# Performance work log

Hardware: AMD Instinct MI355X
Metric: run time of the kernel (lower is better)

## Reference

```python
import jax, jax.numpy as jnp
import numpy as np


def setup_inputs() -> dict:
    key = jax.random.key(0)
    k1, k2 = jax.random.split(key)
    B, N, M = 4, 16384, 4096
    src_points = jax.random.normal(k1, (B, N, 3), dtype=jnp.float32)
    target_verts = jax.random.normal(k2, (B, M, 3), dtype=jnp.float32)
    return {"src_points": src_points, "target_verts": target_verts}


def reference(src_points, target_verts):
    # target_faces=None path of ChamferLoss: degenerate one-vertex triangles,
    # so closest-point-on-mesh == nearest target vertex.
    # d2[b,n,m] = ||p_bn - v_bm||^2 via the expansion p2 + v2 - 2 p.v
    p2 = jnp.sum(src_points * src_points, axis=-1)          # (B, N)
    v2 = jnp.sum(target_verts * target_verts, axis=-1)      # (B, M)
    pv = jnp.einsum('bnd,bmd->bnm', src_points, target_verts)  # (B, N, M)
    d2 = p2[:, :, None] + v2[:, None, :] - 2.0 * pv
    d2 = jnp.maximum(d2, 0.0)
    min_d2 = jnp.min(d2, axis=-1)                            # (B, N)
    num_src_per_batch = src_points.shape[1]
    loss = jnp.sum(min_d2, axis=-1) / num_src_per_batch      # (B,)
    return loss
```

## Files before the change

### kernel.cpp

```cpp
#include <hip/hip_runtime.h>
#include <float.h>


typedef __bf16 bf16x8 __attribute__((ext_vector_type(8)));
typedef float  f32x16 __attribute__((ext_vector_type(16)));

constexpr int B = 4, N = 16384, M = 4096;
constexpr int BN = B * N;
constexpr int NCHUNK = 4;
constexpr int CHUNK_V = M / NCHUNK;
constexpr int TILES = CHUNK_V / 32;
constexpr int TPB = 256;
constexpr int PPB = 128;
constexpr int PBLK = BN / PPB;
constexpr size_t BFRAG_BYTES = (size_t)B * M * 32;

__global__ __launch_bounds__(256) void chamfer_pre(
    const float* __restrict__ tv, unsigned char* __restrict__ bfr,
    float* __restrict__ out)
{
    if (blockIdx.x == 0 && threadIdx.x < B) out[threadIdx.x] = 0.0f;
    int i = blockIdx.x * 256 + threadIdx.x;
    int b = i >> 12;
    int m = i & (M - 1);
    float x = tv[3 * i + 0], y = tv[3 * i + 1], z = tv[3 * i + 2];
    __bf16 xh = (__bf16)x, yh = (__bf16)y, zh = (__bf16)z;
    float xhf = (float)xh, yhf = (float)yh, zhf = (float)zh;
    __bf16 xl = (__bf16)(x - xhf), yl = (__bf16)(y - yhf), zl = (__bf16)(z - zhf);
    float v2 = fmaf(x, x, fmaf(y, y, z * z));
    __bf16 v2h = (__bf16)v2;
    __bf16 v2l = (__bf16)(v2 - (float)v2h);
    __bf16 zero = (__bf16)0.0f;

    bf16x8 h0, h1;
    h0[0] = (__bf16)(-2.0f * xhf); h0[1] = (__bf16)(-2.0f * yhf);
    h0[2] = (__bf16)(-2.0f * zhf);
    h0[3] = h0[0]; h0[4] = h0[1]; h0[5] = h0[2];
    h0[6] = (__bf16)(-2.0f * (float)xl); h0[7] = (__bf16)(-2.0f * (float)yl);
    h1[0] = (__bf16)(-2.0f * (float)zl); h1[1] = v2h; h1[2] = v2l;
    h1[3] = zero; h1[4] = zero; h1[5] = zero; h1[6] = zero; h1[7] = zero;

    int chunk = m >> 10, local = m & (CHUNK_V - 1), tile = local >> 5, c = m & 31;
    size_t base = (size_t)b * 131072 + (size_t)chunk * 32768 + tile * 1024 + c * 16;
    *(bf16x8*)(bfr + base)       = h0;
    *(bf16x8*)(bfr + base + 512) = h1;
}

__global__ __launch_bounds__(TPB, 4) void chamfer_mfma(
    const float* __restrict__ src, const unsigned char* __restrict__ bfr,
    float* __restrict__ partial)
{
    __shared__ uint4 lds4[2048];
    const char* ldsc = (const char*)lds4;
    const int blk   = blockIdx.x;
    const int chunk = blk & 3;
    const int pblk  = blk >> 2;
    const int b     = pblk >> 7;
    const int t     = threadIdx.x;
    const int w     = t >> 6, L = t & 63;
    const int half  = L >> 5, c = L & 31;

    const uint4* gsrc = (const uint4*)(bfr + (size_t)b * 131072 + (size_t)chunk * 32768);
#pragma unroll
    for (int i = 0; i < 8; ++i) lds4[i * 256 + t] = gsrc[i * 256 + t];

    const int gp = pblk * PPB + w * 32 + c;
    float ax = src[3*gp], ay = src[3*gp+1], az = src[3*gp+2];
    __bf16 one = (__bf16)1.0f, zero = (__bf16)0.0f;
    bf16x8 aA;
    {
        __bf16 xh=(__bf16)ax, yh=(__bf16)ay, zh=(__bf16)az;
        __bf16 xl=(__bf16)(ax-(float)xh), yl=(__bf16)(ay-(float)yh), zl=(__bf16)(az-(float)zh);
        if (half == 0) { aA[0]=xh; aA[1]=yh; aA[2]=zh; aA[3]=xl; aA[4]=yl; aA[5]=zl; aA[6]=xh; aA[7]=yh; }
        else { aA[0]=zh; aA[1]=one; aA[2]=one; aA[3]=zero; aA[4]=zero; aA[5]=zero; aA[6]=zero; aA[7]=zero; }
    }

    f32x16 mn, zeroC;
#pragma unroll
    for (int r = 0; r < 16; ++r) { mn[r] = FLT_MAX; zeroC[r] = 0.0f; }

    __syncthreads();

    const int laneoff = half * 512 + c * 16;
#pragma unroll 4
    for (int tl = 0; tl < TILES; ++tl) {
        bf16x8 bf = *(const bf16x8*)(ldsc + tl * 1024 + laneoff);
        f32x16 C = __builtin_amdgcn_mfma_f32_32x32x16_bf16(aA, bf, zeroC, 0, 0, 0);
#pragma unroll
        for (int r = 0; r < 16; ++r) mn[r] = fminf(mn[r], C[r]);
    }

#pragma unroll
    for (int off = 16; off > 0; off >>= 1) {
#pragma unroll
        for (int r = 0; r < 16; ++r)
            mn[r] = fminf(mn[r], __shfl_xor(mn[r], off, 64));
    }
    float* pout = partial + (size_t)chunk * BN + pblk * PPB + w * 32;
#pragma unroll
    for (int r = 0; r < 16; ++r) {
        int row = (r & 3) + 8 * (r >> 2) + 4 * half;
        if (c == row) pout[row] = mn[r];
    }
}

__global__ __launch_bounds__(256) void chamfer_reduce(
    const float* __restrict__ partial, const float* __restrict__ src,
    float* __restrict__ out)
{
    const int p = blockIdx.x * 256 + threadIdx.x;
    const int b = blockIdx.x >> 6;
    float m = fminf(fminf(partial[p], partial[(size_t)BN + p]),
                    fminf(partial[2 * (size_t)BN + p], partial[3 * (size_t)BN + p]));
    float x = src[3*p], y = src[3*p+1], z = src[3*p+2];
    float pp = fmaf(x, x, fmaf(y, y, z * z));
    float sum = fmaxf(m + pp, 0.0f);

    for (int off = 32; off > 0; off >>= 1)
        sum += __shfl_down(sum, off, 64);
    __shared__ float acc[4];
    if ((threadIdx.x & 63) == 0) acc[threadIdx.x >> 6] = sum;
    __syncthreads();
    if (threadIdx.x == 0) {
        float s = acc[0] + acc[1] + acc[2] + acc[3];
        atomicAdd(&out[b], s * (1.0f / N));
    }
}

extern "C" void kernel_launch(void* const* d_in, const int* in_sizes, int n_in,
                              void* d_out, int out_size, void* d_ws, size_t ws_size,
                              hipStream_t stream) {
    const float* src = (const float*)d_in[0];
    const float* tv  = (const float*)d_in[1];
    float* out = (float*)d_out;
    unsigned char* bfr = (unsigned char*)d_ws;
    float* partial = (float*)((char*)d_ws + BFRAG_BYTES);

    chamfer_pre   <<<(B * M) / 256, 256, 0, stream>>>(tv, bfr, out);
    chamfer_mfma  <<<PBLK * NCHUNK, TPB, 0, stream>>>(src, bfr, partial);
    chamfer_reduce<<<BN / 256, 256, 0, stream>>>(partial, src, out);
}
```

Measured before the change: 77.04 us.

## Fuse preprocessing, MFMA min-search and reduction into one kernel

```diff
diff --git a/kernel.cpp b/kernel.cpp
--- a/kernel.cpp
+++ b/kernel.cpp
@@ -6,24 +6,16 @@
 typedef float  f32x16 __attribute__((ext_vector_type(16)));
 
 constexpr int B = 4, N = 16384, M = 4096;
-constexpr int BN = B * N;
-constexpr int NCHUNK = 4;
-constexpr int CHUNK_V = M / NCHUNK;
-constexpr int TILES = CHUNK_V / 32;
 constexpr int TPB = 256;
 constexpr int PPB = 128;
-constexpr int PBLK = BN / PPB;
-constexpr size_t BFRAG_BYTES = (size_t)B * M * 32;
+constexpr int NBLK = (B * N) / PPB;
+constexpr int PHASES = 8;
+constexpr int PHASE_V = M / PHASES;
+constexpr int PHASE_TILES = PHASE_V / 32;
+constexpr unsigned POISON = 0xAAAAAAAAu;
 
-__global__ __launch_bounds__(256) void chamfer_pre(
-    const float* __restrict__ tv, unsigned char* __restrict__ bfr,
-    float* __restrict__ out)
-{
-    if (blockIdx.x == 0 && threadIdx.x < B) out[threadIdx.x] = 0.0f;
-    int i = blockIdx.x * 256 + threadIdx.x;
-    int b = i >> 12;
-    int m = i & (M - 1);
-    float x = tv[3 * i + 0], y = tv[3 * i + 1], z = tv[3 * i + 2];
+__device__ __forceinline__ void write_vert(char* bp, int u,
+                                           float x, float y, float z) {
     __bf16 xh = (__bf16)x, yh = (__bf16)y, zh = (__bf16)z;
     float xhf = (float)xh, yhf = (float)yh, zhf = (float)zh;
     __bf16 xl = (__bf16)(x - xhf), yl = (__bf16)(y - yhf), zl = (__bf16)(z - zhf);
@@ -31,7 +23,6 @@
     __bf16 v2h = (__bf16)v2;
     __bf16 v2l = (__bf16)(v2 - (float)v2h);
     __bf16 zero = (__bf16)0.0f;
-
     bf16x8 h0, h1;
     h0[0] = (__bf16)(-2.0f * xhf); h0[1] = (__bf16)(-2.0f * yhf);
     h0[2] = (__bf16)(-2.0f * zhf);
@@ -39,38 +30,34 @@
     h0[6] = (__bf16)(-2.0f * (float)xl); h0[7] = (__bf16)(-2.0f * (float)yl);
     h1[0] = (__bf16)(-2.0f * (float)zl); h1[1] = v2h; h1[2] = v2l;
     h1[3] = zero; h1[4] = zero; h1[5] = zero; h1[6] = zero; h1[7] = zero;
-
-    int chunk = m >> 10, local = m & (CHUNK_V - 1), tile = local >> 5, c = m & 31;
-    size_t base = (size_t)b * 131072 + (size_t)chunk * 32768 + tile * 1024 + c * 16;
-    *(bf16x8*)(bfr + base)       = h0;
-    *(bf16x8*)(bfr + base + 512) = h1;
+    char* base = bp + ((u >> 5) << 10) + ((u & 31) << 4);
+    *(bf16x8*)base         = h0;
+    *(bf16x8*)(base + 512) = h1;
 }
 
-__global__ __launch_bounds__(TPB, 4) void chamfer_mfma(
-    const float* __restrict__ src, const unsigned char* __restrict__ bfr,
-    float* __restrict__ partial)
+__global__ __launch_bounds__(TPB, 2) void chamfer_fused(
+    const float* __restrict__ src, const float* __restrict__ tv,
+    float* __restrict__ out, float* __restrict__ ws)
 {
-    __shared__ uint4 lds4[2048];
-    const char* ldsc = (const char*)lds4;
-    const int blk   = blockIdx.x;
-    const int chunk = blk & 3;
-    const int pblk  = blk >> 2;
-    const int b     = pblk >> 7;
-    const int t     = threadIdx.x;
-    const int w     = t >> 6, L = t & 63;
-    const int half  = L >> 5, c = L & 31;
+    __shared__ char buf[2][PHASE_TILES * 1024];
+    __shared__ float acc[4];
+    __shared__ int flag;
 
-    const uint4* gsrc = (const uint4*)(bfr + (size_t)b * 131072 + (size_t)chunk * 32768);
-#pragma unroll
-    for (int i = 0; i < 8; ++i) lds4[i * 256 + t] = gsrc[i * 256 + t];
+    const int blk  = blockIdx.x;
+    const int b    = blk >> 7;
+    const int t    = threadIdx.x;
+    const int w    = t >> 6, L = t & 63;
+    const int half = L >> 5, c = L & 31;
 
-    const int gp = pblk * PPB + w * 32 + c;
-    float ax = src[3*gp], ay = src[3*gp+1], az = src[3*gp+2];
+    const int gp = blk * PPB + w * 32 + c;
+    float ax = src[3 * gp], ay = src[3 * gp + 1], az = src[3 * gp + 2];
+    float pp = fmaf(ax, ax, fmaf(ay, ay, az * az));
     __bf16 one = (__bf16)1.0f, zero = (__bf16)0.0f;
     bf16x8 aA;
     {
-        __bf16 xh=(__bf16)ax, yh=(__bf16)ay, zh=(__bf16)az;
-        __bf16 xl=(__bf16)(ax-(float)xh), yl=(__bf16)(ay-(float)yh), zl=(__bf16)(az-(float)zh);
+        __bf16 xh = (__bf16)ax, yh = (__bf16)ay, zh = (__bf16)az;
+        __bf16 xl = (__bf16)(ax - (float)xh), yl = (__bf16)(ay - (float)yh),
+               zl = (__bf16)(az - (float)zh);
         if (half == 0) { aA[0]=xh; aA[1]=yh; aA[2]=zh; aA[3]=xl; aA[4]=yl; aA[5]=zl; aA[6]=xh; aA[7]=yh; }
         else { aA[0]=zh; aA[1]=one; aA[2]=one; aA[3]=zero; aA[4]=zero; aA[5]=zero; aA[6]=zero; aA[7]=zero; }
     }
@@ -79,15 +66,34 @@
 #pragma unroll
     for (int r = 0; r < 16; ++r) { mn[r] = FLT_MAX; zeroC[r] = 0.0f; }
 
-    __syncthreads();
+    const float* tvb = tv + (size_t)b * M * 3;
+    float r0, r1, r2, r3, r4, r5;
+    {
+        const float* p = tvb + 6 * t;
+        float2 A = *(const float2*)p, Bq = *(const float2*)(p + 2),
+               Cq = *(const float2*)(p + 4);
+        r0 = A.x; r1 = A.y; r2 = Bq.x; r3 = Bq.y; r4 = Cq.x; r5 = Cq.y;
+    }
 
-    const int laneoff = half * 512 + c * 16;
+    for (int phase = 0; phase < PHASES; ++phase) {
+        char* bp = buf[phase & 1];
+        write_vert(bp, 2 * t,     r0, r1, r2);
+        write_vert(bp, 2 * t + 1, r3, r4, r5);
+        if (phase + 1 < PHASES) {
+            const float* p = tvb + (size_t)(phase + 1) * PHASE_V * 3 + 6 * t;
+            float2 A = *(const float2*)p, Bq = *(const float2*)(p + 2),
+                   Cq = *(const float2*)(p + 4);
+            r0 = A.x; r1 = A.y; r2 = Bq.x; r3 = Bq.y; r4 = Cq.x; r5 = Cq.y;
+        }
+        __syncthreads();
+        const char* rp = bp + half * 512 + c * 16;
 #pragma unroll 4
-    for (int tl = 0; tl < TILES; ++tl) {
-        bf16x8 bf = *(const bf16x8*)(ldsc + tl * 1024 + laneoff);
-        f32x16 C = __builtin_amdgcn_mfma_f32_32x32x16_bf16(aA, bf, zeroC, 0, 0, 0);
+        for (int tl = 0; tl < PHASE_TILES; ++tl) {
+            bf16x8 bf = *(const bf16x8*)(rp + tl * 1024);
+            f32x16 C = __builtin_amdgcn_mfma_f32_32x32x16_bf16(aA, bf, zeroC, 0, 0, 0);
 #pragma unroll
-        for (int r = 0; r < 16; ++r) mn[r] = fminf(mn[r], C[r]);
+            for (int r = 0; r < 16; ++r) mn[r] = fminf(mn[r], C[r]);
+        }
     }
 
 #pragma unroll
@@ -96,34 +102,35 @@
         for (int r = 0; r < 16; ++r)
             mn[r] = fminf(mn[r], __shfl_xor(mn[r], off, 64));
     }
-    float* pout = partial + (size_t)chunk * BN + pblk * PPB + w * 32;
+    float s = 0.0f;
 #pragma unroll
     for (int r = 0; r < 16; ++r) {
         int row = (r & 3) + 8 * (r >> 2) + 4 * half;
-        if (c == row) pout[row] = mn[r];
+        if (c == row) s = fmaxf(mn[r] + pp, 0.0f);
     }
-}
+    for (int off = 32; off > 0; off >>= 1)
+        s += __shfl_down(s, off, 64);
+    if (L == 0) acc[w] = s;
+    __syncthreads();
 
-__global__ __launch_bounds__(256) void chamfer_reduce(
-    const float* __restrict__ partial, const float* __restrict__ src,
-    float* __restrict__ out)
-{
-    const int p = blockIdx.x * 256 + threadIdx.x;
-    const int b = blockIdx.x >> 6;
-    float m = fminf(fminf(partial[p], partial[(size_t)BN + p]),
-                    fminf(partial[2 * (size_t)BN + p], partial[3 * (size_t)BN + p]));
-    float x = src[3*p], y = src[3*p+1], z = src[3*p+2];
-    float pp = fmaf(x, x, fmaf(y, y, z * z));
-    float sum = fmaxf(m + pp, 0.0f);
+    if (t == 0) {
+        float bs = acc[0] + acc[1] + acc[2] + acc[3];
+        unsigned* cnt = (unsigned*)(ws + NBLK);
+        atomicExch(&ws[blk], bs);
+        __threadfence();
+        (void)atomicCAS(cnt, POISON, 0u);
+        __threadfence();
+        unsigned n = atomicAdd(cnt, 1u);
+        flag = (n == NBLK - 1) ? 1 : 0;
+    }
+    __syncthreads();
 
-    for (int off = 32; off > 0; off >>= 1)
-        sum += __shfl_down(sum, off, 64);
-    __shared__ float acc[4];
-    if ((threadIdx.x & 63) == 0) acc[threadIdx.x >> 6] = sum;
-    __syncthreads();
-    if (threadIdx.x == 0) {
-        float s = acc[0] + acc[1] + acc[2] + acc[3];
-        atomicAdd(&out[b], s * (1.0f / N));
+    if (flag) {
+        float s2 = atomicAdd(&ws[w * 128 + L], 0.0f)
+                 + atomicAdd(&ws[w * 128 + 64 + L], 0.0f);
+        for (int off = 32; off > 0; off >>= 1)
+            s2 += __shfl_down(s2, off, 64);
+        if (L == 0) out[w] = s2 * (1.0f / N);
     }
 }
 
@@ -133,10 +140,7 @@
     const float* src = (const float*)d_in[0];
     const float* tv  = (const float*)d_in[1];
     float* out = (float*)d_out;
-    unsigned char* bfr = (unsigned char*)d_ws;
-    float* partial = (float*)((char*)d_ws + BFRAG_BYTES);
+    float* ws  = (float*)d_ws;
 
-    chamfer_pre   <<<(B * M) / 256, 256, 0, stream>>>(tv, bfr, out);
-    chamfer_mfma  <<<PBLK * NCHUNK, TPB, 0, stream>>>(src, bfr, partial);
-    chamfer_reduce<<<BN / 256, 256, 0, stream>>>(partial, src, out);
+    chamfer_fused<<<NBLK, TPB, 0, stream>>>(src, tv, out, ws);
 }
```

Result: slower. 80.69 us (+4.7%).

## Swap MFMA operand roles so point min reduces in-lane, and split vertices into 8 chunks

Applied to the files above, without the earlier changes.

```diff
diff --git a/kernel.cpp b/kernel.cpp
--- a/kernel.cpp
+++ b/kernel.cpp
@@ -7,7 +7,7 @@
 
 constexpr int B = 4, N = 16384, M = 4096;
 constexpr int BN = B * N;
-constexpr int NCHUNK = 4;
+constexpr int NCHUNK = 8;
 constexpr int CHUNK_V = M / NCHUNK;
 constexpr int TILES = CHUNK_V / 32;
 constexpr int TPB = 256;
@@ -21,7 +21,6 @@
 {
     if (blockIdx.x == 0 && threadIdx.x < B) out[threadIdx.x] = 0.0f;
     int i = blockIdx.x * 256 + threadIdx.x;
-    int b = i >> 12;
     int m = i & (M - 1);
     float x = tv[3 * i + 0], y = tv[3 * i + 1], z = tv[3 * i + 2];
     __bf16 xh = (__bf16)x, yh = (__bf16)y, zh = (__bf16)z;
@@ -40,81 +39,81 @@
     h1[0] = (__bf16)(-2.0f * (float)zl); h1[1] = v2h; h1[2] = v2l;
     h1[3] = zero; h1[4] = zero; h1[5] = zero; h1[6] = zero; h1[7] = zero;
 
-    int chunk = m >> 10, local = m & (CHUNK_V - 1), tile = local >> 5, c = m & 31;
-    size_t base = (size_t)b * 131072 + (size_t)chunk * 32768 + tile * 1024 + c * 16;
+    int chunk = m >> 9, local = m & (CHUNK_V - 1), tile = local >> 5, r = m & 31;
+    size_t base = (size_t)(i >> 12) * 131072 + (size_t)chunk * 16384
+                + tile * 1024 + r * 16;
     *(bf16x8*)(bfr + base)       = h0;
     *(bf16x8*)(bfr + base + 512) = h1;
 }
 
-__global__ __launch_bounds__(TPB, 4) void chamfer_mfma(
+__global__ __launch_bounds__(TPB) void chamfer_mfma(
     const float* __restrict__ src, const unsigned char* __restrict__ bfr,
     float* __restrict__ partial)
 {
-    __shared__ uint4 lds4[2048];
+    __shared__ uint4 lds4[1024];
     const char* ldsc = (const char*)lds4;
     const int blk   = blockIdx.x;
-    const int chunk = blk & 3;
-    const int pblk  = blk >> 2;
+    const int chunk = blk & 7;
+    const int pblk  = blk >> 3;
     const int b     = pblk >> 7;
     const int t     = threadIdx.x;
     const int w     = t >> 6, L = t & 63;
     const int half  = L >> 5, c = L & 31;
 
-    const uint4* gsrc = (const uint4*)(bfr + (size_t)b * 131072 + (size_t)chunk * 32768);
+    const uint4* gsrc = (const uint4*)(bfr + (size_t)b * 131072 + (size_t)chunk * 16384);
 #pragma unroll
-    for (int i = 0; i < 8; ++i) lds4[i * 256 + t] = gsrc[i * 256 + t];
+    for (int i = 0; i < 4; ++i) lds4[i * 256 + t] = gsrc[i * 256 + t];
 
     const int gp = pblk * PPB + w * 32 + c;
-    float ax = src[3*gp], ay = src[3*gp+1], az = src[3*gp+2];
+    float ax = src[3 * gp], ay = src[3 * gp + 1], az = src[3 * gp + 2];
+    float pp = fmaf(ax, ax, fmaf(ay, ay, az * az));
     __bf16 one = (__bf16)1.0f, zero = (__bf16)0.0f;
-    bf16x8 aA;
+    bf16x8 bP;
     {
-        __bf16 xh=(__bf16)ax, yh=(__bf16)ay, zh=(__bf16)az;
-        __bf16 xl=(__bf16)(ax-(float)xh), yl=(__bf16)(ay-(float)yh), zl=(__bf16)(az-(float)zh);
-        if (half == 0) { aA[0]=xh; aA[1]=yh; aA[2]=zh; aA[3]=xl; aA[4]=yl; aA[5]=zl; aA[6]=xh; aA[7]=yh; }
-        else { aA[0]=zh; aA[1]=one; aA[2]=one; aA[3]=zero; aA[4]=zero; aA[5]=zero; aA[6]=zero; aA[7]=zero; }
+        __bf16 xh = (__bf16)ax, yh = (__bf16)ay, zh = (__bf16)az;
+        __bf16 xl = (__bf16)(ax - (float)xh), yl = (__bf16)(ay - (float)yh),
+               zl = (__bf16)(az - (float)zh);
+        if (half == 0) { bP[0]=xh; bP[1]=yh; bP[2]=zh; bP[3]=xl; bP[4]=yl; bP[5]=zl; bP[6]=xh; bP[7]=yh; }
+        else { bP[0]=zh; bP[1]=one; bP[2]=one; bP[3]=zero; bP[4]=zero; bP[5]=zero; bP[6]=zero; bP[7]=zero; }
     }
 
-    f32x16 mn, zeroC;
+    float mn[8];
+    f32x16 zeroC;
 #pragma unroll
-    for (int r = 0; r < 16; ++r) { mn[r] = FLT_MAX; zeroC[r] = 0.0f; }
+    for (int u = 0; u < 8; ++u) mn[u] = FLT_MAX;
+#pragma unroll
+    for (int r = 0; r < 16; ++r) zeroC[r] = 0.0f;
 
     __syncthreads();
 
     const int laneoff = half * 512 + c * 16;
 #pragma unroll 4
     for (int tl = 0; tl < TILES; ++tl) {
-        bf16x8 bf = *(const bf16x8*)(ldsc + tl * 1024 + laneoff);
-        f32x16 C = __builtin_amdgcn_mfma_f32_32x32x16_bf16(aA, bf, zeroC, 0, 0, 0);
+        bf16x8 av = *(const bf16x8*)(ldsc + tl * 1024 + laneoff);
+        f32x16 C = __builtin_amdgcn_mfma_f32_32x32x16_bf16(av, bP, zeroC, 0, 0, 0);
 #pragma unroll
-        for (int r = 0; r < 16; ++r) mn[r] = fminf(mn[r], C[r]);
+        for (int u = 0; u < 8; ++u)
+            mn[u] = fminf(fminf(mn[u], C[2 * u]), C[2 * u + 1]);
     }
 
-#pragma unroll
-    for (int off = 16; off > 0; off >>= 1) {
-#pragma unroll
-        for (int r = 0; r < 16; ++r)
-            mn[r] = fminf(mn[r], __shfl_xor(mn[r], off, 64));
-    }
-    float* pout = partial + (size_t)chunk * BN + pblk * PPB + w * 32;
-#pragma unroll
-    for (int r = 0; r < 16; ++r) {
-        int row = (r & 3) + 8 * (r >> 2) + 4 * half;
-        if (c == row) pout[row] = mn[r];
-    }
+    float m01 = fminf(fminf(mn[0], mn[1]), fminf(mn[2], mn[3]));
+    float m23 = fminf(fminf(mn[4], mn[5]), fminf(mn[6], mn[7]));
+    float m = fminf(m01, m23);
+    m = fminf(m, __shfl_xor(m, 32, 64));
+    if (L < 32)
+        partial[(size_t)chunk * BN + gp] = m + pp;
 }
 
 __global__ __launch_bounds__(256) void chamfer_reduce(
-    const float* __restrict__ partial, const float* __restrict__ src,
-    float* __restrict__ out)
+    const float* __restrict__ partial, float* __restrict__ out)
 {
     const int p = blockIdx.x * 256 + threadIdx.x;
     const int b = blockIdx.x >> 6;
-    float m = fminf(fminf(partial[p], partial[(size_t)BN + p]),
-                    fminf(partial[2 * (size_t)BN + p], partial[3 * (size_t)BN + p]));
-    float x = src[3*p], y = src[3*p+1], z = src[3*p+2];
-    float pp = fmaf(x, x, fmaf(y, y, z * z));
-    float sum = fmaxf(m + pp, 0.0f);
+    float m = FLT_MAX;
+#pragma unroll
+    for (int cgr = 0; cgr < NCHUNK; ++cgr)
+        m = fminf(m, partial[(size_t)cgr * BN + p]);
+    float sum = fmaxf(m, 0.0f);
 
     for (int off = 32; off > 0; off >>= 1)
         sum += __shfl_down(sum, off, 64);
@@ -138,5 +137,5 @@
 
     chamfer_pre   <<<(B * M) / 256, 256, 0, stream>>>(tv, bfr, out);
     chamfer_mfma  <<<PBLK * NCHUNK, TPB, 0, stream>>>(src, bfr, partial);
-    chamfer_reduce<<<BN / 256, 256, 0, stream>>>(partial, src, out);
+    chamfer_reduce<<<BN / 256, 256, 0, stream>>>(partial, out);
 }
```

After: 74.18 us (median of 2 runs). 3.7% less time.
